# Performance work log

Hardware: AMD Instinct MI355X
Metric: run time of the kernel (lower is better)

The kernel has to match this reference:

```python
import jax, jax.numpy as jnp
import numpy as np

# Static multi-scale pyramid (H, W per level); Nv = sum(H*W) = 13294
SPATIAL = np.array([[100, 100], [50, 50], [25, 25], [13, 13]], dtype=np.int64)
B, C, NH, NL, NP = 2, 256, 8, 4, 4
D = C // NH
TOT = NH * NL * NP


def setup_inputs() -> dict:
    key = jax.random.key(0)
    ks = jax.random.split(key, 10)
    Nv = int((SPATIAL[:, 0] * SPATIAL[:, 1]).sum())
    Nq = Nv
    query = jax.random.normal(ks[0], (B, Nq, C), dtype=jnp.float32)
    value = jax.random.normal(ks[1], (B, Nv, C), dtype=jnp.float32)
    reference_points = jax.random.uniform(ks[2], (B, Nq, NL, 2), minval=0.05, maxval=0.95, dtype=jnp.float32)
    spatial_shapes = jnp.asarray(SPATIAL)
    level_start_index = jnp.asarray(np.concatenate([[0], np.cumsum(SPATIAL[:, 0] * SPATIAL[:, 1])[:-1]]))
    # sampling_offsets: small random weight + the rotated-grid bias from _reset_parameters
    W_off = 0.01 * jax.random.normal(ks[3], (C, TOT * 2), dtype=jnp.float32)
    thetas = np.arange(NH, dtype=np.float64) * (2.0 * np.pi / NH)
    grid = np.stack([np.cos(thetas), np.sin(thetas)], -1)
    grid = grid / np.abs(grid).max(-1, keepdims=True)
    grid = np.tile(grid[:, None, None, :], (1, NL, NP, 1)) * (np.arange(NP) + 1)[None, None, :, None]
    b_off = jnp.asarray(grid.reshape(-1), dtype=jnp.float32)
    W_attn = 0.01 * jax.random.normal(ks[4], (C, TOT), dtype=jnp.float32)
    b_attn = jnp.zeros((TOT,), jnp.float32)
    W_val = jax.random.normal(ks[5], (C, C), dtype=jnp.float32) / np.sqrt(C)
    b_val = jnp.zeros((C,), jnp.float32)
    W_out = jax.random.normal(ks[6], (C, C), dtype=jnp.float32) / np.sqrt(C)
    b_out = jnp.zeros((C,), jnp.float32)
    return {"query": query, "value": value, "reference_points": reference_points,
            "spatial_shapes": spatial_shapes, "level_start_index": level_start_index,
            "W_off": W_off, "b_off": b_off, "W_attn": W_attn, "b_attn": b_attn,
            "W_val": W_val, "b_val": b_val, "W_out": W_out, "b_out": b_out}


def _bilinear(vl, loc, H, W):
    # vl: [B, h, H*W, D]; loc: [B, Nq, h, P, 2] normalized (x, y) in [0,1]
    # Matches F.grid_sample(mode='bilinear', padding_mode='zeros', align_corners=False)
    Bb, h, _, Dd = vl.shape
    Nq, P = loc.shape[1], loc.shape[3]
    x = loc[..., 0] * W - 0.5
    y = loc[..., 1] * H - 0.5
    x0 = jnp.floor(x)
    y0 = jnp.floor(y)
    fx = x - x0
    fy = y - y0
    out = jnp.zeros((Bb, h, Nq * P, Dd), vl.dtype)
    corners = ((0, 0, (1 - fx) * (1 - fy)), (1, 0, fx * (1 - fy)),
               (0, 1, (1 - fx) * fy), (1, 1, fx * fy))
    for dx, dy, w in corners:
        xi = x0 + dx
        yi = y0 + dy
        valid = (xi >= 0) & (xi < W) & (yi >= 0) & (yi < H)
        idx = (jnp.clip(yi, 0, H - 1) * W + jnp.clip(xi, 0, W - 1)).astype(jnp.int32)
        idx = idx.transpose(0, 2, 1, 3).reshape(Bb, h, Nq * P)          # [B,h,Nq*P]
        wv = (w * valid).transpose(0, 2, 1, 3).reshape(Bb, h, Nq * P)   # [B,h,Nq*P]
        g = jnp.take_along_axis(vl, idx[..., None], axis=2)             # [B,h,Nq*P,D]
        out = out + g * wv[..., None]
    return out.reshape(Bb, h, Nq, P, Dd)


def reference(query, value, reference_points, spatial_shapes, level_start_index,
              W_off, b_off, W_attn, b_attn, W_val, b_val, W_out, b_out):
    Bb, Nq, Cc = query.shape
    v = (value @ W_val + b_val).reshape(Bb, -1, NH, D)                  # [B,Nv,h,D]
    off = (query @ W_off + b_off).reshape(Bb, Nq, NH, NL, NP, 2)
    attn = jax.nn.softmax((query @ W_attn + b_attn).reshape(Bb, Nq, NH, NL * NP), axis=-1)
    attn = attn.reshape(Bb, Nq, NH, NL, NP)
    # offset normalizer is (W, H) per level
    norm = jnp.asarray(SPATIAL[:, ::-1].copy(), dtype=query.dtype)      # [L,2]
    loc = reference_points[:, :, None, :, None, :] + off / norm[None, None, None, :, None, :]
    starts = np.concatenate([[0], np.cumsum(SPATIAL[:, 0] * SPATIAL[:, 1])])
    out_acc = jnp.zeros((Bb, NH, Nq, D), query.dtype)
    for l in range(NL):
        H, W = int(SPATIAL[l, 0]), int(SPATIAL[l, 1])
        vl = v[:, int(starts[l]):int(starts[l + 1])].transpose(0, 2, 1, 3)  # [B,h,HW,D]
        samp = _bilinear(vl, loc[:, :, :, l], H, W)                     # [B,h,Nq,P,D]
        w_l = attn[:, :, :, l].transpose(0, 2, 1, 3)                    # [B,h,Nq,P]
        out_acc = out_acc + jnp.einsum('bhqpd,bhqp->bhqd', samp, w_l)
    out = out_acc.transpose(0, 2, 1, 3).reshape(Bb, Nq, Cc)
    return out @ W_out + b_out
```

## Files before the change

### kernel.cpp

```cpp
#include <hip/hip_runtime.h>
#include <hip/hip_bf16.h>

#define NQ  13294
#define NV  13294
#define BQ  26588

typedef __attribute__((ext_vector_type(8))) short short8;
typedef __attribute__((ext_vector_type(4))) float f32x4;

static __device__ __forceinline__ ushort f2bf(float f) {
    unsigned int x = __float_as_uint(f);
    unsigned int r = (x + 0x7fffu + ((x >> 16) & 1u)) >> 16;
    return (ushort)r;
}
static __device__ __forceinline__ uint cvtpk_bf16(float a, float b) {
    uint r;
    asm("v_cvt_pk_bf16_f32 %0, %1, %2" : "=v"(r) : "v"(a), "v"(b));
    return r;
}
static __device__ __forceinline__ uint cvtpk_f16(float a, float b) {
    uint r;
    asm("v_cvt_pkrtz_f16_f32 %0, %1, %2" : "=v"(r) : "v"(a), "v"(b));
    return r;
}
static __device__ __forceinline__ float f16lo(uint u) {
    _Float16 h; ushort t = (ushort)(u & 0xffffu);
    __builtin_memcpy(&h, &t, 2); return (float)h;
}
static __device__ __forceinline__ float f16hi(uint u) {
    _Float16 h; ushort t = (ushort)(u >> 16);
    __builtin_memcpy(&h, &t, 2); return (float)h;
}
static __device__ __forceinline__ float fmamix_ll(float acc, uint g, uint w) {
    asm("v_fma_mix_f32 %0, %1, %2, %0 op_sel:[0,0,0] op_sel_hi:[1,1,0]" : "+v"(acc) : "v"(g), "v"(w));
    return acc;
}
static __device__ __forceinline__ float fmamix_hl(float acc, uint g, uint w) {
    asm("v_fma_mix_f32 %0, %1, %2, %0 op_sel:[1,0,0] op_sel_hi:[1,1,0]" : "+v"(acc) : "v"(g), "v"(w));
    return acc;
}
static __device__ __forceinline__ float fmamix_lh(float acc, uint g, uint w) {
    asm("v_fma_mix_f32 %0, %1, %2, %0 op_sel:[0,1,0] op_sel_hi:[1,1,0]" : "+v"(acc) : "v"(g), "v"(w));
    return acc;
}
static __device__ __forceinline__ float fmamix_hh(float acc, uint g, uint w) {
    asm("v_fma_mix_f32 %0, %1, %2, %0 op_sel:[1,1,0] op_sel_hi:[1,1,0]" : "+v"(acc) : "v"(g), "v"(w));
    return acc;
}

__global__ __launch_bounds__(256) void prep_weights(
    const float* __restrict__ Wv, const float* __restrict__ Wo,
    const float* __restrict__ Wa, const float* __restrict__ Wu,
    const float* __restrict__ bo, const float* __restrict__ ba,
    ushort* __restrict__ tWv, ushort* __restrict__ tWoa,
    ushort* __restrict__ tWu, float* __restrict__ boa) {
    const int blk = blockIdx.x;
    const int tid = threadIdx.x;
    if (blk == 56) {
        if (tid < 256) boa[tid] = bo[tid];
        int j = tid + 256;
        if (j < 384) boa[j] = ba[j - 256];
        return;
    }
    __shared__ float t[64][65];
    const float* src; ushort* dst; int srcN, k0, n0, drow0;
    if (blk < 16)      { int u = blk;      src = Wv; srcN = 256; dst = tWv;  k0 = (u >> 2) * 64; n0 = (u & 3) * 64; drow0 = n0; }
    else if (blk < 32) { int u = blk - 16; src = Wo; srcN = 256; dst = tWoa; k0 = (u >> 2) * 64; n0 = (u & 3) * 64; drow0 = n0; }
    else if (blk < 40) { int u = blk - 32; src = Wa; srcN = 128; dst = tWoa; k0 = (u >> 1) * 64; n0 = (u & 1) * 64; drow0 = 256 + n0; }
    else               { int u = blk - 40; src = Wu; srcN = 256; dst = tWu;  k0 = (u >> 2) * 64; n0 = (u & 3) * 64; drow0 = n0; }
#pragma unroll
    for (int it = 0; it < 16; ++it) {
        int idx = tid + it * 256, r = idx >> 6, c = idx & 63;
        t[r][c] = src[(size_t)(k0 + r) * srcN + n0 + c];
    }
    __syncthreads();
#pragma unroll
    for (int it = 0; it < 16; ++it) {
        int idx = tid + it * 256, r = idx >> 6, c = idx & 63;
        dst[(size_t)(drow0 + r) * 256 + k0 + c] = f2bf(t[c][r]);
    }
}

#define LDP 40
#define ABUF (64 * LDP)
#define BBUF (128 * LDP)

template<int AF32>
static __device__ __forceinline__ void gemm_core5(
    const void* __restrict__ Aptr, const ushort* __restrict__ Bt,
    const float* __restrict__ bias, void* __restrict__ Cout,
    int M, int N, int out_mode, int mblk, int nblk,
    ushort* sA, ushort* sB) {
    const int tid = threadIdx.x;
    const int wid = tid >> 6;
    const int lane = tid & 63;
    const int row0 = mblk * 64;
    const int col0 = nblk * 128;
    const int wr = (wid >> 1) * 32;
    const int wc = (wid & 1) * 64;

    f32x4 acc[2][4];
#pragma unroll
    for (int m = 0; m < 2; ++m)
#pragma unroll
        for (int n = 0; n < 4; ++n) acc[m][n] = (f32x4){0.f, 0.f, 0.f, 0.f};

    const int r0 = tid >> 2;
    const int seg = tid & 3;

    float4 rf[2];
    uint4  ra;
    uint4  rb[2];

    auto REGLOAD = [&](int t) {
        int kk = t * 32;
        int gr = row0 + r0; gr = gr < M ? gr : M - 1;
        if (AF32) {
            const float* Af = (const float*)Aptr + (size_t)gr * 256 + kk + seg * 8;
            rf[0] = *reinterpret_cast<const float4*>(Af);
            rf[1] = *reinterpret_cast<const float4*>(Af + 4);
        } else {
            ra = *reinterpret_cast<const uint4*>((const ushort*)Aptr + (size_t)gr * 256 + kk + seg * 8);
        }
        rb[0] = *reinterpret_cast<const uint4*>(Bt + (size_t)(col0 + r0) * 256 + kk + seg * 8);
        rb[1] = *reinterpret_cast<const uint4*>(Bt + (size_t)(col0 + r0 + 64) * 256 + kk + seg * 8);
    };
    auto STORE = [&](int buf) {
        uint4 wa;
        if (AF32) {
            wa.x = cvtpk_bf16(rf[0].x, rf[0].y);
            wa.y = cvtpk_bf16(rf[0].z, rf[0].w);
            wa.z = cvtpk_bf16(rf[1].x, rf[1].y);
            wa.w = cvtpk_bf16(rf[1].z, rf[1].w);
        } else {
            wa = ra;
        }
        *reinterpret_cast<uint4*>(&sA[buf * ABUF + r0 * LDP + seg * 8]) = wa;
        *reinterpret_cast<uint4*>(&sB[buf * BBUF + r0 * LDP + seg * 8]) = rb[0];
        *reinterpret_cast<uint4*>(&sB[buf * BBUF + (r0 + 64) * LDP + seg * 8]) = rb[1];
    };
    auto COMPUTE = [&](int buf) {
        const int rbase = lane & 15;
        const int g8 = (lane >> 4) * 8;
        short8 a[2], b[4];
#pragma unroll
        for (int m = 0; m < 2; ++m)
            a[m] = *reinterpret_cast<const short8*>(&sA[buf * ABUF + (wr + m * 16 + rbase) * LDP + g8]);
#pragma unroll
        for (int n = 0; n < 4; ++n)
            b[n] = *reinterpret_cast<const short8*>(&sB[buf * BBUF + (wc + n * 16 + rbase) * LDP + g8]);
#pragma unroll
        for (int m = 0; m < 2; ++m)
#pragma unroll
            for (int n = 0; n < 4; ++n)
                acc[m][n] = __builtin_amdgcn_mfma_f32_16x16x32_bf16(a[m], b[n], acc[m][n], 0, 0, 0);
    };

    REGLOAD(0);
    STORE(0);
#pragma unroll
    for (int t = 0; t < 8; ++t) {
        __syncthreads();
        if (t < 7) REGLOAD(t + 1);
        COMPUTE(t & 1);
        if (t < 7) STORE((t + 1) & 1);
    }

    const int lr = (lane >> 4) * 4;
    const int lc = lane & 15;
#pragma unroll
    for (int m = 0; m < 2; ++m) {
#pragma unroll
        for (int n = 0; n < 4; ++n) {
            int gcol = col0 + wc + n * 16 + lc;
            float bv = bias[gcol];
#pragma unroll
            for (int j = 0; j < 4; ++j) {
                int grow = row0 + wr + m * 16 + lr + j;
                if (grow < M) {
                    float vv = acc[m][n][j] + bv;
                    if (out_mode == 0) {
                        ((float*)Cout)[(size_t)grow * N + gcol] = vv;
                    } else if (out_mode == 2) {
                        ((ushort*)Cout)[(size_t)grow * N + gcol] = (ushort)(cvtpk_f16(vv, vv) & 0xffffu);
                    } else {
                        int bb = grow >= NV;
                        int pix = grow - bb * NV;
                        int h = gcol >> 5, ch = gcol & 31;
                        ((ushort*)Cout)[(((size_t)(bb * 8 + h)) * NV + pix) * 32 + ch] =
                            (ushort)(cvtpk_f16(vv, vv) & 0xffffu);
                    }
                }
            }
        }
    }
}

__global__ __launch_bounds__(256, 4) void gemm_fused(
    const float* __restrict__ value, const float* __restrict__ query,
    const ushort* __restrict__ tWv, const ushort* __restrict__ tWoa,
    const float* __restrict__ bval, const float* __restrict__ boa,
    ushort* __restrict__ vproj_t, ushort* __restrict__ offattn) {
    __shared__ ushort sA[2 * ABUF];
    __shared__ ushort sB[2 * BBUF];
    const bool g1 = blockIdx.y < 2;
    gemm_core5<1>(g1 ? (const void*)value : (const void*)query,
                  g1 ? tWv : tWoa, g1 ? bval : boa,
                  g1 ? (void*)vproj_t : (void*)offattn,
                  BQ, g1 ? 256 : 384, g1 ? 3 : 2,
                  blockIdx.x, g1 ? blockIdx.y : blockIdx.y - 2, sA, sB);
}

__global__ __launch_bounds__(256, 4) void gemm_out(
    const ushort* __restrict__ outacc, const ushort* __restrict__ tWu,
    const float* __restrict__ bout, float* __restrict__ dout) {
    __shared__ ushort sA[2 * ABUF];
    __shared__ ushort sB[2 * BBUF];
    gemm_core5<0>(outacc, tWu, bout, dout, BQ, 256, 0, blockIdx.x, blockIdx.y, sA, sB);
}

__global__ __launch_bounds__(256, 4) void msda_sample(
    const ushort* __restrict__ offattn,
    const float* __restrict__ refp,
    const ushort* __restrict__ vt,
    ushort* __restrict__ out_acc) {
    __shared__ int2 s_ad[4][256];
    __shared__ uint s_w[4][256];

    const int tid = threadIdx.x;
    const int qi = tid >> 6;
    const int lane = tid & 63;
    const int bq = blockIdx.x * 4 + qi;
    const int b = bq / NQ;
    const int q = bq - b * NQ;
    const int h = lane >> 3;

    const ushort* oa = offattn + (size_t)bq * 384;
    const int t0 = lane * 2;
    uint lgu = *reinterpret_cast<const uint*>(oa + 256 + t0);
    float lg0 = f16lo(lgu), lg1 = f16hi(lgu);
    float m = fmaxf(lg0, lg1);
    m = fmaxf(m, __shfl_xor(m, 1));
    m = fmaxf(m, __shfl_xor(m, 2));
    m = fmaxf(m, __shfl_xor(m, 4));
    float e0 = __expf(lg0 - m), e1 = __expf(lg1 - m);
    float ssum = e0 + e1;
    ssum += __shfl_xor(ssum, 1);
    ssum += __shfl_xor(ssum, 2);
    ssum += __shfl_xor(ssum, 4);
    float inv = 1.f / ssum;

    uint2 offu = *reinterpret_cast<const uint2*>(oa + 2 * t0);
    const int l = (t0 >> 2) & 3;
    const int   Wi = (l == 0) ? 100 : (l == 1) ? 50 : (l == 2) ? 25 : 13;
    const int   st = (l == 0) ? 0 : (l == 1) ? 10000 : (l == 2) ? 12500 : 13125;
    const float Wf = (float)Wi;
    float rx = refp[(((size_t)b * NQ + q) * 4 + l) * 2 + 0];
    float ry = refp[(((size_t)b * NQ + q) * 4 + l) * 2 + 1];
    const int vbase = (b * 8 + h) * NV * 64;

#pragma unroll
    for (int j = 0; j < 2; ++j) {
        float e = (j ? e1 : e0) * inv;
        float ox = j ? f16lo(offu.y) : f16lo(offu.x);
        float oy = j ? f16hi(offu.y) : f16hi(offu.x);
        float x = fmaf(rx, Wf, ox) - 0.5f;
        float y = fmaf(ry, Wf, oy) - 0.5f;
        float x0f = floorf(x), y0f = floorf(y);
        float fx = x - x0f, fy = y - y0f;
        int x0 = (int)x0f, y0 = (int)y0f;
        float wx0 = (x0 >= 0 && x0 < Wi)         ? e * (1.f - fx) : 0.f;
        float wx1 = (x0 + 1 >= 0 && x0 + 1 < Wi) ? e * fx         : 0.f;
        float wy0 = (y0 >= 0 && y0 < Wi)         ? (1.f - fy) : 0.f;
        float wy1 = (y0 + 1 >= 0 && y0 + 1 < Wi) ? fy         : 0.f;
        int px0 = min(max(x0, 0), Wi - 1) * 64;
        int px1 = min(max(x0 + 1, 0), Wi - 1) * 64;
        int a0 = vbase + (st + min(max(y0, 0), Wi - 1) * Wi) * 64;
        int a1 = vbase + (st + min(max(y0 + 1, 0), Wi - 1) * Wi) * 64;
        int s = 2 * (lane & 7) + j;
        int u = ((s ^ h) << 4) + (h << 1);
        s_ad[qi][u]     = make_int2(a0 + px0, a1 + px0);
        s_ad[qi][u + 1] = make_int2(a0 + px1, a1 + px1);
        s_w[qi][u]      = cvtpk_f16(wx0 * wy0, wx0 * wy1);
        s_w[qi][u + 1]  = cvtpk_f16(wx1 * wy0, wx1 * wy1);
    }
    __syncthreads();

    const int xbit = (lane >> 2) & 1;
    const int cg16 = (lane & 3) * 16;
    const char* vtc = (const char*)vt;

    int2 A[16]; uint Wp[16];
#pragma unroll
    for (int ss = 0; ss < 16; ++ss) {
        int u = ((ss ^ h) << 4) + (h << 1) + xbit;
        int2 a = s_ad[qi][u];
        A[ss] = make_int2(a.x + cg16, a.y + cg16);
        Wp[ss] = s_w[qi][u];
    }

    float acc[8] = {0.f, 0.f, 0.f, 0.f, 0.f, 0.f, 0.f, 0.f};
#pragma unroll
    for (int ss = 0; ss < 16; ++ss) {
        uint4 g0 = *reinterpret_cast<const uint4*>(vtc + (uint)A[ss].x);
        uint4 g1 = *reinterpret_cast<const uint4*>(vtc + (uint)A[ss].y);
        uint w = Wp[ss];
        acc[0] = fmamix_ll(acc[0], g0.x, w); acc[1] = fmamix_hl(acc[1], g0.x, w);
        acc[2] = fmamix_ll(acc[2], g0.y, w); acc[3] = fmamix_hl(acc[3], g0.y, w);
        acc[4] = fmamix_ll(acc[4], g0.z, w); acc[5] = fmamix_hl(acc[5], g0.z, w);
        acc[6] = fmamix_ll(acc[6], g0.w, w); acc[7] = fmamix_hl(acc[7], g0.w, w);
        acc[0] = fmamix_lh(acc[0], g1.x, w); acc[1] = fmamix_hh(acc[1], g1.x, w);
        acc[2] = fmamix_lh(acc[2], g1.y, w); acc[3] = fmamix_hh(acc[3], g1.y, w);
        acc[4] = fmamix_lh(acc[4], g1.z, w); acc[5] = fmamix_hh(acc[5], g1.z, w);
        acc[6] = fmamix_lh(acc[6], g1.w, w); acc[7] = fmamix_hh(acc[7], g1.w, w);
    }

#pragma unroll
    for (int i = 0; i < 8; ++i) acc[i] += __shfl_xor(acc[i], 4);
    if (xbit == 0) {
        uint4 o;
        o.x = cvtpk_bf16(acc[0], acc[1]);
        o.y = cvtpk_bf16(acc[2], acc[3]);
        o.z = cvtpk_bf16(acc[4], acc[5]);
        o.w = cvtpk_bf16(acc[6], acc[7]);
        *reinterpret_cast<uint4*>(out_acc + (size_t)bq * 256 + h * 32 + (lane & 3) * 8) = o;
    }
}

extern "C" void kernel_launch(void* const* d_in, const int* in_sizes, int n_in,
                              void* d_out, int out_size, void* d_ws, size_t ws_size,
                              hipStream_t stream) {
    const float* query  = (const float*)d_in[0];
    const float* value  = (const float*)d_in[1];
    const float* refp   = (const float*)d_in[2];
    const float* W_off  = (const float*)d_in[5];
    const float* b_off  = (const float*)d_in[6];
    const float* W_attn = (const float*)d_in[7];
    const float* b_attn = (const float*)d_in[8];
    const float* W_val  = (const float*)d_in[9];
    const float* b_val  = (const float*)d_in[10];
    const float* W_out  = (const float*)d_in[11];
    const float* b_out  = (const float*)d_in[12];

    const size_t ROWB = (size_t)BQ * 256 * 2;
    char* ws = (char*)d_ws;
    ushort* vproj_t = (ushort*)(ws);
    ushort* outacc  = (ushort*)(ws + ROWB);
    ushort* offattn = (ushort*)(ws + 2 * ROWB);
    char*   wbase   = ws + 2 * ROWB + (size_t)BQ * 384 * 2;
    ushort* tWv  = (ushort*)(wbase);
    ushort* tWoa = tWv + 65536;
    ushort* tWu  = tWoa + 98304;
    float*  boa  = (float*)(tWu + 65536);

    prep_weights<<<57, 256, 0, stream>>>(
        W_val, W_off, W_attn, W_out, b_off, b_attn, tWv, tWoa, tWu, boa);

    gemm_fused<<<dim3(416, 5), 256, 0, stream>>>(
        value, query, tWv, tWoa, b_val, boa, vproj_t, offattn);

    msda_sample<<<BQ / 4, 256, 0, stream>>>(offattn, refp, vproj_t, outacc);

    gemm_out<<<dim3(416, 2), 256, 0, stream>>>(outacc, tWu, b_out, (float*)d_out);
}
```

Measured before the change: 102.5 us.

## Fuse deformable sampling with output projection GEMM in one kernel

Merges the sampling kernel and the output projection GEMM into a single kernel. Each block samples 64 query rows into shared memory as fp16, then multiplies them by the fp16 output weights using MFMA. This removes the round trip of the intermediate accumulator through global memory and one kernel launch. In exchange, each block loops serially over 16 rows per wave with a barrier inside the loop, the launch drops to 416 blocks, B operands are read straight from global memory, and the output weights and intermediate switch from bf16 to fp16.

```diff
diff --git a/kernel.cpp b/kernel.cpp
--- a/kernel.cpp
+++ b/kernel.cpp
@@ -7,6 +7,7 @@
 
 typedef __attribute__((ext_vector_type(8))) short short8;
 typedef __attribute__((ext_vector_type(4))) float f32x4;
+typedef _Float16 half8 __attribute__((ext_vector_type(8)));
 
 static __device__ __forceinline__ ushort f2bf(float f) {
     unsigned int x = __float_as_uint(f);
@@ -63,11 +64,11 @@
         return;
     }
     __shared__ float t[64][65];
-    const float* src; ushort* dst; int srcN, k0, n0, drow0;
+    const float* src; ushort* dst; int srcN, k0, n0, drow0; bool as_f16 = false;
     if (blk < 16)      { int u = blk;      src = Wv; srcN = 256; dst = tWv;  k0 = (u >> 2) * 64; n0 = (u & 3) * 64; drow0 = n0; }
     else if (blk < 32) { int u = blk - 16; src = Wo; srcN = 256; dst = tWoa; k0 = (u >> 2) * 64; n0 = (u & 3) * 64; drow0 = n0; }
     else if (blk < 40) { int u = blk - 32; src = Wa; srcN = 128; dst = tWoa; k0 = (u >> 1) * 64; n0 = (u & 1) * 64; drow0 = 256 + n0; }
-    else               { int u = blk - 40; src = Wu; srcN = 256; dst = tWu;  k0 = (u >> 2) * 64; n0 = (u & 3) * 64; drow0 = n0; }
+    else               { int u = blk - 40; src = Wu; srcN = 256; dst = tWu;  k0 = (u >> 2) * 64; n0 = (u & 3) * 64; drow0 = n0; as_f16 = true; }
 #pragma unroll
     for (int it = 0; it < 16; ++it) {
         int idx = tid + it * 256, r = idx >> 6, c = idx & 63;
@@ -77,7 +78,9 @@
 #pragma unroll
     for (int it = 0; it < 16; ++it) {
         int idx = tid + it * 256, r = idx >> 6, c = idx & 63;
-        dst[(size_t)(drow0 + r) * 256 + k0 + c] = f2bf(t[c][r]);
+        float v = t[c][r];
+        dst[(size_t)(drow0 + r) * 256 + k0 + c] =
+            as_f16 ? (ushort)(cvtpk_f16(v, v) & 0xffffu) : f2bf(v);
     }
 }
 
@@ -85,9 +88,8 @@
 #define ABUF (64 * LDP)
 #define BBUF (128 * LDP)
 
-template<int AF32>
 static __device__ __forceinline__ void gemm_core5(
-    const void* __restrict__ Aptr, const ushort* __restrict__ Bt,
+    const float* __restrict__ Aptr, const ushort* __restrict__ Bt,
     const float* __restrict__ bias, void* __restrict__ Cout,
     int M, int N, int out_mode, int mblk, int nblk,
     ushort* sA, ushort* sB) {
@@ -109,32 +111,23 @@
     const int seg = tid & 3;
 
     float4 rf[2];
-    uint4  ra;
     uint4  rb[2];
 
     auto REGLOAD = [&](int t) {
         int kk = t * 32;
         int gr = row0 + r0; gr = gr < M ? gr : M - 1;
-        if (AF32) {
-            const float* Af = (const float*)Aptr + (size_t)gr * 256 + kk + seg * 8;
-            rf[0] = *reinterpret_cast<const float4*>(Af);
-            rf[1] = *reinterpret_cast<const float4*>(Af + 4);
-        } else {
-            ra = *reinterpret_cast<const uint4*>((const ushort*)Aptr + (size_t)gr * 256 + kk + seg * 8);
-        }
+        const float* Af = Aptr + (size_t)gr * 256 + kk + seg * 8;
+        rf[0] = *reinterpret_cast<const float4*>(Af);
+        rf[1] = *reinterpret_cast<const float4*>(Af + 4);
         rb[0] = *reinterpret_cast<const uint4*>(Bt + (size_t)(col0 + r0) * 256 + kk + seg * 8);
         rb[1] = *reinterpret_cast<const uint4*>(Bt + (size_t)(col0 + r0 + 64) * 256 + kk + seg * 8);
     };
     auto STORE = [&](int buf) {
         uint4 wa;
-        if (AF32) {
-            wa.x = cvtpk_bf16(rf[0].x, rf[0].y);
-            wa.y = cvtpk_bf16(rf[0].z, rf[0].w);
-            wa.z = cvtpk_bf16(rf[1].x, rf[1].y);
-            wa.w = cvtpk_bf16(rf[1].z, rf[1].w);
-        } else {
-            wa = ra;
-        }
+        wa.x = cvtpk_bf16(rf[0].x, rf[0].y);
+        wa.y = cvtpk_bf16(rf[0].z, rf[0].w);
+        wa.z = cvtpk_bf16(rf[1].x, rf[1].y);
+        wa.w = cvtpk_bf16(rf[1].z, rf[1].w);
         *reinterpret_cast<uint4*>(&sA[buf * ABUF + r0 * LDP + seg * 8]) = wa;
         *reinterpret_cast<uint4*>(&sB[buf * BBUF + r0 * LDP + seg * 8]) = rb[0];
         *reinterpret_cast<uint4*>(&sB[buf * BBUF + (r0 + 64) * LDP + seg * 8]) = rb[1];
@@ -179,9 +172,7 @@
                 int grow = row0 + wr + m * 16 + lr + j;
                 if (grow < M) {
                     float vv = acc[m][n][j] + bv;
-                    if (out_mode == 0) {
-                        ((float*)Cout)[(size_t)grow * N + gcol] = vv;
-                    } else if (out_mode == 2) {
+                    if (out_mode == 2) {
                         ((ushort*)Cout)[(size_t)grow * N + gcol] = (ushort)(cvtpk_f16(vv, vv) & 0xffffu);
                     } else {
                         int bb = grow >= NV;
@@ -204,126 +195,172 @@
     __shared__ ushort sA[2 * ABUF];
     __shared__ ushort sB[2 * BBUF];
     const bool g1 = blockIdx.y < 2;
-    gemm_core5<1>(g1 ? (const void*)value : (const void*)query,
-                  g1 ? tWv : tWoa, g1 ? bval : boa,
-                  g1 ? (void*)vproj_t : (void*)offattn,
-                  BQ, g1 ? 256 : 384, g1 ? 3 : 2,
-                  blockIdx.x, g1 ? blockIdx.y : blockIdx.y - 2, sA, sB);
-}
-
-__global__ __launch_bounds__(256, 4) void gemm_out(
-    const ushort* __restrict__ outacc, const ushort* __restrict__ tWu,
-    const float* __restrict__ bout, float* __restrict__ dout) {
-    __shared__ ushort sA[2 * ABUF];
-    __shared__ ushort sB[2 * BBUF];
-    gemm_core5<0>(outacc, tWu, bout, dout, BQ, 256, 0, blockIdx.x, blockIdx.y, sA, sB);
-}
-
-__global__ __launch_bounds__(256, 4) void msda_sample(
+    gemm_core5(g1 ? value : query,
+               g1 ? tWv : tWoa, g1 ? bval : boa,
+               g1 ? (void*)vproj_t : (void*)offattn,
+               BQ, g1 ? 256 : 384, g1 ? 3 : 2,
+               blockIdx.x, g1 ? blockIdx.y : blockIdx.y - 2, sA, sB);
+}
+
+#define AROW 264
+__global__ __launch_bounds__(256, 3) void msda_out(
     const ushort* __restrict__ offattn,
     const float* __restrict__ refp,
     const ushort* __restrict__ vt,
-    ushort* __restrict__ out_acc) {
+    const ushort* __restrict__ tWu,
+    const float* __restrict__ bout,
+    float* __restrict__ dout) {
+    __shared__ ushort sA[64 * AROW];
     __shared__ int2 s_ad[4][256];
     __shared__ uint s_w[4][256];
 
     const int tid = threadIdx.x;
-    const int qi = tid >> 6;
+    const int wid = tid >> 6;
     const int lane = tid & 63;
-    const int bq = blockIdx.x * 4 + qi;
-    const int b = bq / NQ;
-    const int q = bq - b * NQ;
+    const int row0 = blockIdx.x * 64;
     const int h = lane >> 3;
 
-    const ushort* oa = offattn + (size_t)bq * 384;
-    const int t0 = lane * 2;
-    uint lgu = *reinterpret_cast<const uint*>(oa + 256 + t0);
-    float lg0 = f16lo(lgu), lg1 = f16hi(lgu);
-    float m = fmaxf(lg0, lg1);
-    m = fmaxf(m, __shfl_xor(m, 1));
-    m = fmaxf(m, __shfl_xor(m, 2));
-    m = fmaxf(m, __shfl_xor(m, 4));
-    float e0 = __expf(lg0 - m), e1 = __expf(lg1 - m);
-    float ssum = e0 + e1;
-    ssum += __shfl_xor(ssum, 1);
-    ssum += __shfl_xor(ssum, 2);
-    ssum += __shfl_xor(ssum, 4);
-    float inv = 1.f / ssum;
-
-    uint2 offu = *reinterpret_cast<const uint2*>(oa + 2 * t0);
-    const int l = (t0 >> 2) & 3;
-    const int   Wi = (l == 0) ? 100 : (l == 1) ? 50 : (l == 2) ? 25 : 13;
-    const int   st = (l == 0) ? 0 : (l == 1) ? 10000 : (l == 2) ? 12500 : 13125;
-    const float Wf = (float)Wi;
-    float rx = refp[(((size_t)b * NQ + q) * 4 + l) * 2 + 0];
-    float ry = refp[(((size_t)b * NQ + q) * 4 + l) * 2 + 1];
-    const int vbase = (b * 8 + h) * NV * 64;
-
-#pragma unroll
-    for (int j = 0; j < 2; ++j) {
-        float e = (j ? e1 : e0) * inv;
-        float ox = j ? f16lo(offu.y) : f16lo(offu.x);
-        float oy = j ? f16hi(offu.y) : f16hi(offu.x);
-        float x = fmaf(rx, Wf, ox) - 0.5f;
-        float y = fmaf(ry, Wf, oy) - 0.5f;
-        float x0f = floorf(x), y0f = floorf(y);
-        float fx = x - x0f, fy = y - y0f;
-        int x0 = (int)x0f, y0 = (int)y0f;
-        float wx0 = (x0 >= 0 && x0 < Wi)         ? e * (1.f - fx) : 0.f;
-        float wx1 = (x0 + 1 >= 0 && x0 + 1 < Wi) ? e * fx         : 0.f;
-        float wy0 = (y0 >= 0 && y0 < Wi)         ? (1.f - fy) : 0.f;
-        float wy1 = (y0 + 1 >= 0 && y0 + 1 < Wi) ? fy         : 0.f;
-        int px0 = min(max(x0, 0), Wi - 1) * 64;
-        int px1 = min(max(x0 + 1, 0), Wi - 1) * 64;
-        int a0 = vbase + (st + min(max(y0, 0), Wi - 1) * Wi) * 64;
-        int a1 = vbase + (st + min(max(y0 + 1, 0), Wi - 1) * Wi) * 64;
-        int s = 2 * (lane & 7) + j;
-        int u = ((s ^ h) << 4) + (h << 1);
-        s_ad[qi][u]     = make_int2(a0 + px0, a1 + px0);
-        s_ad[qi][u + 1] = make_int2(a0 + px1, a1 + px1);
-        s_w[qi][u]      = cvtpk_f16(wx0 * wy0, wx0 * wy1);
-        s_w[qi][u + 1]  = cvtpk_f16(wx1 * wy0, wx1 * wy1);
+    for (int qq = 0; qq < 16; ++qq) {
+        const int r = wid * 16 + qq;
+        int bq = row0 + r; if (bq >= BQ) bq = BQ - 1;
+        const int b = bq / NQ;
+        const int q = bq - b * NQ;
+
+        const ushort* oa = offattn + (size_t)bq * 384;
+        const int t0 = lane * 2;
+        uint lgu = *reinterpret_cast<const uint*>(oa + 256 + t0);
+        float lg0 = f16lo(lgu), lg1 = f16hi(lgu);
+        float m = fmaxf(lg0, lg1);
+        m = fmaxf(m, __shfl_xor(m, 1));
+        m = fmaxf(m, __shfl_xor(m, 2));
+        m = fmaxf(m, __shfl_xor(m, 4));
+        float e0 = __expf(lg0 - m), e1 = __expf(lg1 - m);
+        float ssum = e0 + e1;
+        ssum += __shfl_xor(ssum, 1);
+        ssum += __shfl_xor(ssum, 2);
+        ssum += __shfl_xor(ssum, 4);
+        float inv = 1.f / ssum;
+
+        uint2 offu = *reinterpret_cast<const uint2*>(oa + 2 * t0);
+        const int l = (t0 >> 2) & 3;
+        const int   Wi = (l == 0) ? 100 : (l == 1) ? 50 : (l == 2) ? 25 : 13;
+        const int   st = (l == 0) ? 0 : (l == 1) ? 10000 : (l == 2) ? 12500 : 13125;
+        const float Wf = (float)Wi;
+        float rx = refp[(((size_t)b * NQ + q) * 4 + l) * 2 + 0];
+        float ry = refp[(((size_t)b * NQ + q) * 4 + l) * 2 + 1];
+        const int vbase = (b * 8 + h) * NV * 64;
+
+#pragma unroll
+        for (int j = 0; j < 2; ++j) {
+            float e = (j ? e1 : e0) * inv;
+            float ox = j ? f16lo(offu.y) : f16lo(offu.x);
+            float oy = j ? f16hi(offu.y) : f16hi(offu.x);
+            float x = fmaf(rx, Wf, ox) - 0.5f;
+            float y = fmaf(ry, Wf, oy) - 0.5f;
+            float x0f = floorf(x), y0f = floorf(y);
+            float fx = x - x0f, fy = y - y0f;
+            int x0 = (int)x0f, y0 = (int)y0f;
+            float wx0 = (x0 >= 0 && x0 < Wi)         ? e * (1.f - fx) : 0.f;
+            float wx1 = (x0 + 1 >= 0 && x0 + 1 < Wi) ? e * fx         : 0.f;
+            float wy0 = (y0 >= 0 && y0 < Wi)         ? (1.f - fy) : 0.f;
+            float wy1 = (y0 + 1 >= 0 && y0 + 1 < Wi) ? fy         : 0.f;
+            int px0 = min(max(x0, 0), Wi - 1) * 64;
+            int px1 = min(max(x0 + 1, 0), Wi - 1) * 64;
+            int a0 = vbase + (st + min(max(y0, 0), Wi - 1) * Wi) * 64;
+            int a1 = vbase + (st + min(max(y0 + 1, 0), Wi - 1) * Wi) * 64;
+            int s = 2 * (lane & 7) + j;
+            int u = ((s ^ h) << 4) + (h << 1);
+            s_ad[wid][u]     = make_int2(a0 + px0, a1 + px0);
+            s_ad[wid][u + 1] = make_int2(a0 + px1, a1 + px1);
+            s_w[wid][u]      = cvtpk_f16(wx0 * wy0, wx0 * wy1);
+            s_w[wid][u + 1]  = cvtpk_f16(wx1 * wy0, wx1 * wy1);
+        }
+        __syncthreads();
+
+        const int xbit = (lane >> 2) & 1;
+        const int cg16 = (lane & 3) * 16;
+        const char* vtc = (const char*)vt;
+
+        int2 A[16]; uint Wp[16];
+#pragma unroll
+        for (int ss = 0; ss < 16; ++ss) {
+            int u = ((ss ^ h) << 4) + (h << 1) + xbit;
+            int2 a = s_ad[wid][u];
+            A[ss] = make_int2(a.x + cg16, a.y + cg16);
+            Wp[ss] = s_w[wid][u];
+        }
+
+        float acc[8] = {0.f, 0.f, 0.f, 0.f, 0.f, 0.f, 0.f, 0.f};
+#pragma unroll
+        for (int ss = 0; ss < 16; ++ss) {
+            uint4 g0 = *reinterpret_cast<const uint4*>(vtc + (uint)A[ss].x);
+            uint4 g1 = *reinterpret_cast<const uint4*>(vtc + (uint)A[ss].y);
+            uint w = Wp[ss];
+            acc[0] = fmamix_ll(acc[0], g0.x, w); acc[1] = fmamix_hl(acc[1], g0.x, w);
+            acc[2] = fmamix_ll(acc[2], g0.y, w); acc[3] = fmamix_hl(acc[3], g0.y, w);
+            acc[4] = fmamix_ll(acc[4], g0.z, w); acc[5] = fmamix_hl(acc[5], g0.z, w);
+            acc[6] = fmamix_ll(acc[6], g0.w, w); acc[7] = fmamix_hl(acc[7], g0.w, w);
+            acc[0] = fmamix_lh(acc[0], g1.x, w); acc[1] = fmamix_hh(acc[1], g1.x, w);
+            acc[2] = fmamix_lh(acc[2], g1.y, w); acc[3] = fmamix_hh(acc[3], g1.y, w);
+            acc[4] = fmamix_lh(acc[4], g1.z, w); acc[5] = fmamix_hh(acc[5], g1.z, w);
+            acc[6] = fmamix_lh(acc[6], g1.w, w); acc[7] = fmamix_hh(acc[7], g1.w, w);
+        }
+
+#pragma unroll
+        for (int i = 0; i < 8; ++i) acc[i] += __shfl_xor(acc[i], 4);
+        if (xbit == 0) {
+            uint4 o;
+            o.x = cvtpk_f16(acc[0], acc[1]);
+            o.y = cvtpk_f16(acc[2], acc[3]);
+            o.z = cvtpk_f16(acc[4], acc[5]);
+            o.w = cvtpk_f16(acc[6], acc[7]);
+            *reinterpret_cast<uint4*>(&sA[r * AROW + h * 32 + (lane & 3) * 8]) = o;
+        }
     }
     __syncthreads();
 
-    const int xbit = (lane >> 2) & 1;
-    const int cg16 = (lane & 3) * 16;
-    const char* vtc = (const char*)vt;
-
-    int2 A[16]; uint Wp[16];
-#pragma unroll
-    for (int ss = 0; ss < 16; ++ss) {
-        int u = ((ss ^ h) << 4) + (h << 1) + xbit;
-        int2 a = s_ad[qi][u];
-        A[ss] = make_int2(a.x + cg16, a.y + cg16);
-        Wp[ss] = s_w[qi][u];
-    }
-
-    float acc[8] = {0.f, 0.f, 0.f, 0.f, 0.f, 0.f, 0.f, 0.f};
-#pragma unroll
-    for (int ss = 0; ss < 16; ++ss) {
-        uint4 g0 = *reinterpret_cast<const uint4*>(vtc + (uint)A[ss].x);
-        uint4 g1 = *reinterpret_cast<const uint4*>(vtc + (uint)A[ss].y);
-        uint w = Wp[ss];
-        acc[0] = fmamix_ll(acc[0], g0.x, w); acc[1] = fmamix_hl(acc[1], g0.x, w);
-        acc[2] = fmamix_ll(acc[2], g0.y, w); acc[3] = fmamix_hl(acc[3], g0.y, w);
-        acc[4] = fmamix_ll(acc[4], g0.z, w); acc[5] = fmamix_hl(acc[5], g0.z, w);
-        acc[6] = fmamix_ll(acc[6], g0.w, w); acc[7] = fmamix_hl(acc[7], g0.w, w);
-        acc[0] = fmamix_lh(acc[0], g1.x, w); acc[1] = fmamix_hh(acc[1], g1.x, w);
-        acc[2] = fmamix_lh(acc[2], g1.y, w); acc[3] = fmamix_hh(acc[3], g1.y, w);
-        acc[4] = fmamix_lh(acc[4], g1.z, w); acc[5] = fmamix_hh(acc[5], g1.z, w);
-        acc[6] = fmamix_lh(acc[6], g1.w, w); acc[7] = fmamix_hh(acc[7], g1.w, w);
-    }
-
-#pragma unroll
-    for (int i = 0; i < 8; ++i) acc[i] += __shfl_xor(acc[i], 4);
-    if (xbit == 0) {
-        uint4 o;
-        o.x = cvtpk_bf16(acc[0], acc[1]);
-        o.y = cvtpk_bf16(acc[2], acc[3]);
-        o.z = cvtpk_bf16(acc[4], acc[5]);
-        o.w = cvtpk_bf16(acc[6], acc[7]);
-        *reinterpret_cast<uint4*>(out_acc + (size_t)bq * 256 + h * 32 + (lane & 3) * 8) = o;
+    const int wr = (wid >> 1) * 32;
+    const int wc = (wid & 1) * 128;
+    const int rbase = lane & 15;
+    const int g8 = (lane >> 4) * 8;
+
+    f32x4 acc2[2][8];
+#pragma unroll
+    for (int m = 0; m < 2; ++m)
+#pragma unroll
+        for (int n = 0; n < 8; ++n) acc2[m][n] = (f32x4){0.f, 0.f, 0.f, 0.f};
+
+#pragma unroll
+    for (int kk = 0; kk < 256; kk += 32) {
+        half8 a[2], b[8];
+#pragma unroll
+        for (int m = 0; m < 2; ++m)
+            a[m] = *reinterpret_cast<const half8*>(&sA[(wr + m * 16 + rbase) * AROW + kk + g8]);
+#pragma unroll
+        for (int n = 0; n < 8; ++n)
+            b[n] = *reinterpret_cast<const half8*>(tWu + (size_t)(wc + n * 16 + rbase) * 256 + kk + g8);
+#pragma unroll
+        for (int m = 0; m < 2; ++m)
+#pragma unroll
+            for (int n = 0; n < 8; ++n)
+                acc2[m][n] = __builtin_amdgcn_mfma_f32_16x16x32_f16(a[m], b[n], acc2[m][n], 0, 0, 0);
+    }
+
+    const int lr = (lane >> 4) * 4;
+    const int lc = lane & 15;
+#pragma unroll
+    for (int m = 0; m < 2; ++m) {
+#pragma unroll
+        for (int n = 0; n < 8; ++n) {
+            int gcol = wc + n * 16 + lc;
+            float bv = bout[gcol];
+#pragma unroll
+            for (int j = 0; j < 4; ++j) {
+                int grow = row0 + wr + m * 16 + lr + j;
+                if (grow < BQ)
+                    dout[(size_t)grow * 256 + gcol] = acc2[m][n][j] + bv;
+            }
+        }
     }
 }
 
@@ -345,9 +382,8 @@
     const size_t ROWB = (size_t)BQ * 256 * 2;
     char* ws = (char*)d_ws;
     ushort* vproj_t = (ushort*)(ws);
-    ushort* outacc  = (ushort*)(ws + ROWB);
-    ushort* offattn = (ushort*)(ws + 2 * ROWB);
-    char*   wbase   = ws + 2 * ROWB + (size_t)BQ * 384 * 2;
+    ushort* offattn = (ushort*)(ws + ROWB);
+    char*   wbase   = ws + ROWB + (size_t)BQ * 384 * 2;
     ushort* tWv  = (ushort*)(wbase);
     ushort* tWoa = tWv + 65536;
     ushort* tWu  = tWoa + 98304;
@@ -359,7 +395,5 @@
     gemm_fused<<<dim3(416, 5), 256, 0, stream>>>(
         value, query, tWv, tWoa, b_val, boa, vproj_t, offattn);
 
-    msda_sample<<<BQ / 4, 256, 0, stream>>>(offattn, refp, vproj_t, outacc);
-
-    gemm_out<<<dim3(416, 2), 256, 0, stream>>>(outacc, tWu, b_out, (float*)d_out);
-}
+    msda_out<<<416, 256, 0, stream>>>(offattn, refp, vproj_t, tWu, b_out, (float*)d_out);
+}
```

New measurement: 163.5 us. 1.6x slower.
